# Optimization experiments

Measured on AMD Instinct MI355X. Metric: run time of the kernel, lower is better.

## Reference

```python
import jax, jax.numpy as jnp
import numpy as np

EMB = 512
HEADS = 8
HEAD_DIM = EMB // HEADS


def setup_inputs() -> dict:
    key = jax.random.key(0)
    ks = jax.random.split(key, 6)
    b, t = 2, 4096
    x = jax.random.normal(ks[0], (b, t, EMB), dtype=jnp.float32)
    sc = 1.0 / np.sqrt(HEAD_DIM).astype(np.float32)
    Wq = jax.random.normal(ks[1], (HEAD_DIM, HEAD_DIM), dtype=jnp.float32) * sc
    Wk = jax.random.normal(ks[2], (HEAD_DIM, HEAD_DIM), dtype=jnp.float32) * sc
    Wv = jax.random.normal(ks[3], (HEAD_DIM, HEAD_DIM), dtype=jnp.float32) * sc
    Wu = jax.random.normal(ks[4], (EMB, EMB), dtype=jnp.float32) * (1.0 / np.sqrt(EMB).astype(np.float32))
    bu = jnp.zeros((EMB,), dtype=jnp.float32)
    return {"x": x, "Wq": Wq, "Wk": Wk, "Wv": Wv, "Wu": Wu, "bu": bu}


def reference(x, Wq, Wk, Wv, Wu, bu):
    b, t, e = x.shape
    s = Wq.shape[0]
    h = e // s
    xh = x.reshape(b, t, h, s)
    # torch Linear: y = x @ W.T (no bias for q/k/v)
    q = jnp.einsum('bthd,ed->bthe', xh, Wq)  # e here == s (head dim)
    k = jnp.einsum('bthd,ed->bthe', xh, Wk)
    v = jnp.einsum('bthd,ed->bthe', xh, Wv)
    # full [b,h,t,t] score matrix, scaled by sqrt(emb_dim) as in source
    dot = jnp.einsum('bqhd,bkhd->bhqk', q, k) / (e ** 0.5)
    att = jax.nn.softmax(dot, axis=-1)
    out = jnp.einsum('bhqk,bkhd->bqhd', att, v).reshape(b, t, e)
    return out @ Wu.T + bu
```

## Files before the change

### kernel.cpp

```cpp
#include <hip/hip_runtime.h>
#include <hip/hip_bf16.h>


#define T 4096
#define HEADS 8
#define HD 64
#define EMB 512
#define BATCH 2
#define BH (BATCH * HEADS)
#define NT (T / 64)

typedef __attribute__((ext_vector_type(8))) short short8;
typedef __attribute__((ext_vector_type(4))) short short4v;
typedef __attribute__((ext_vector_type(4))) float floatx4;

__device__ inline short f2bf(float f) {
  union { float f; unsigned u; } v; v.f = f;
  unsigned r = v.u + 0x7FFF + ((v.u >> 16) & 1);
  return (short)(r >> 16);
}

__device__ inline float bf2f(short s) {
  union { unsigned u; float f; } v; v.u = ((unsigned)(unsigned short)s) << 16;
  return v.f;
}

__device__ inline short8 pack8(float4 a, float4 b) {
  union { __hip_bfloat162 h[4]; short8 s; } u;
  float2 t;
  t.x = a.x; t.y = a.y; u.h[0] = __float22bfloat162_rn(t);
  t.x = a.z; t.y = a.w; u.h[1] = __float22bfloat162_rn(t);
  t.x = b.x; t.y = b.y; u.h[2] = __float22bfloat162_rn(t);
  t.x = b.z; t.y = b.w; u.h[3] = __float22bfloat162_rn(t);
  return u.s;
}

__device__ inline short4v pack4(floatx4 a) {
  union { __hip_bfloat162 h[2]; short4v s; } u;
  float2 t;
  t.x = a[0]; t.y = a[1]; u.h[0] = __float22bfloat162_rn(t);
  t.x = a[2]; t.y = a[3]; u.h[1] = __float22bfloat162_rn(t);
  return u.s;
}

__device__ inline short8 packbf(const float* p) {
  union { __hip_bfloat162 h[4]; short8 s; } u;
  float2 t;
  t.x = p[0]; t.y = p[1]; u.h[0] = __float22bfloat162_rn(t);
  t.x = p[2]; t.y = p[3]; u.h[1] = __float22bfloat162_rn(t);
  t.x = p[4]; t.y = p[5]; u.h[2] = __float22bfloat162_rn(t);
  t.x = p[6]; t.y = p[7]; u.h[3] = __float22bfloat162_rn(t);
  return u.s;
}

__device__ inline int swz(int row, int byte) {
  return (row * 128 + byte) ^ ((row & 7) << 4);
}

__device__ inline int swz32(int row, int byte) {
  return (row * 64 + byte) ^ ((row & 3) << 4);
}

__global__ __launch_bounds__(256) void qkv_kernel(
    const float* __restrict__ x, const float* __restrict__ Wq,
    const float* __restrict__ Wk, const float* __restrict__ Wv,
    short* __restrict__ q_ws, short* __restrict__ k_ws, short* __restrict__ vt_ws) {
  __shared__ __align__(16) short xs[128 * 64];
  __shared__ __align__(16) short ob[128 * 64];
  const int tid = threadIdx.x;
  const int lane = tid & 63;
  const int w = tid >> 6;
  const int g = lane >> 4, lr = lane & 15;
  const long rowbase = (long)blockIdx.x * 128;
  const float c2 = 0.0441941738241592f * 1.4426950408889634f;

  {
    int row = tid >> 1, hf = tid & 1;
    const float4* xv = (const float4*)(x + (rowbase + row) * 64 + hf * 32);
#pragma unroll
    for (int c = 0; c < 4; ++c) {
      float4 a = xv[2 * c], b = xv[2 * c + 1];
      *(short8*)((char*)xs + swz(row, hf * 64 + c * 16)) = pack8(a, b);
    }
  }
  __syncthreads();

  const float* Ws[3] = {Wq, Wk, Wv};
  for (int m = 0; m < 3; ++m) {
    const float* W = Ws[m];
    const float sc = (m == 0) ? c2 : 1.0f;
    for (int nt = 0; nt < 4; ++nt) {
      const int coln_a = nt * 16 + lr;
      const float4* wr0 = (const float4*)(W + coln_a * 64 + 8 * g);
      const float4* wr1 = (const float4*)(W + coln_a * 64 + 32 + 8 * g);
      float4 w0 = wr0[0], w1 = wr0[1], w2 = wr1[0], w3 = wr1[1];
      w0.x *= sc; w0.y *= sc; w0.z *= sc; w0.w *= sc;
      w1.x *= sc; w1.y *= sc; w1.z *= sc; w1.w *= sc;
      w2.x *= sc; w2.y *= sc; w2.z *= sc; w2.w *= sc;
      w3.x *= sc; w3.y *= sc; w3.z *= sc; w3.w *= sc;
      short8 b0 = pack8(w0, w1);
      short8 b1 = pack8(w2, w3);
      for (int mr = 0; mr < 2; ++mr) {
        const int arow = w * 32 + mr * 16 + lr;
        short8 a0 = *(short8*)((char*)xs + swz(arow, g * 16));
        short8 a1 = *(short8*)((char*)xs + swz(arow, 64 + g * 16));
        floatx4 acc = 0;
        acc = __builtin_amdgcn_mfma_f32_16x16x32_bf16(b0, a0, acc, 0, 0, 0);
        acc = __builtin_amdgcn_mfma_f32_16x16x32_bf16(b1, a1, acc, 0, 0, 0);
        if (m < 2) {
          *(short4v*)((char*)ob + swz(w * 32 + mr * 16 + lr, 32 * nt + 8 * g)) = pack4(acc);
        } else {
          long R = rowbase + w * 32 + mr * 16 + lr;
          int bb = (int)(R >> 15);
          int h = (int)(R & 7);
          int t = (int)((R >> 3) & 4095);
          int tp = (t & ~31) | (((t >> 2) & 3) << 3) | (((t >> 4) & 1) << 2) | (t & 3);
          short4v pk = pack4(acc);
#pragma unroll
          for (int jj = 0; jj < 4; ++jj) {
            int coln = nt * 16 + 4 * g + jj;
            vt_ws[((long)(bb * HEADS + h) * 64 + coln) * T + tp] = pk[jj];
          }
        }
      }
    }
    if (m < 2) {
      short* dst_ws = (m == 0) ? q_ws : k_ws;
      __syncthreads();
      {
        int row = tid >> 1, hf = tid & 1;
        long R = rowbase + row;
        int bb = (int)(R >> 15);
        int h = (int)(R & 7);
        int t = (int)((R >> 3) & 4095);
        short* dst = dst_ws + ((long)(bb * HEADS + h) * T + t) * 64 + hf * 32;
#pragma unroll
        for (int c = 0; c < 4; ++c) {
          short8 v = *(short8*)((char*)ob + swz(row, hf * 64 + c * 16));
          *(short8*)(dst + c * 8) = v;
        }
      }
      __syncthreads();
    }
  }
}

__global__ __launch_bounds__(256, 4) void attn_kernel(
    const short* __restrict__ q_ws, const short* __restrict__ k_ws,
    const short* __restrict__ vt_ws, short* __restrict__ pacc,
    float* __restrict__ ellw) {
  __shared__ __align__(16) short Ks[32 * 64];
  __shared__ __align__(16) short Vs[64 * 32];
  const int tid = threadIdx.x, lane = tid & 63, w = tid >> 6;
  const int g = lane >> 4, lr = lane & 15;
  const int id = blockIdx.x;
  const int bh = (id & 7) * 2 + ((id >> 3) & 1);
  const int q0 = ((id >> 4) & 31) * 128;
  const int split = (id >> 9) & 3;
  const int kvbase = split * (T / 4);
  const short* Qp = q_ws + (long)bh * T * 64;
  const short* Kp = k_ws + (long)bh * T * 64;
  const short* Vt = vt_ws + (long)bh * 64 * T;

  short8 aq[2][2];
#pragma unroll
  for (int mt = 0; mt < 2; ++mt) {
    int r = q0 + w * 32 + mt * 16 + lr;
    aq[mt][0] = *(const short8*)(Qp + (long)r * 64 + g * 8);
    aq[mt][1] = *(const short8*)(Qp + (long)r * 64 + 32 + g * 8);
  }

  floatx4 acc[2][4];
#pragma unroll
  for (int mt = 0; mt < 2; ++mt)
#pragma unroll
    for (int dt = 0; dt < 4; ++dt) acc[mt][dt] = 0;
  float ellp[2] = {0.f, 0.f};

  const int srowK = tid >> 3;
  const int segK = (tid & 7) * 8;
  const int srowV = tid >> 2;
  const int segV = (tid & 3) * 8;

  {
    short8 k0 = *(const short8*)(Kp + (long)(kvbase + srowK) * 64 + segK);
    short8 v0 = *(const short8*)(Vt + (long)srowV * T + kvbase + segV);
    *(short8*)((char*)Ks + swz(srowK, segK * 2)) = k0;
    *(short8*)((char*)Vs + swz32(srowV, segV * 2)) = v0;
  }
  __syncthreads();

  for (int it = 0; it < 32; ++it) {
    const int nk = kvbase + ((it + 1) & 31) * 32;
    short8 nk0 = *(const short8*)(Kp + (long)(nk + srowK) * 64 + segK);
    short8 nv0 = *(const short8*)(Vt + (long)srowV * T + nk + segV);

    short8 kb[2][2], vb[4];
#pragma unroll
    for (int kt = 0; kt < 2; ++kt) {
      kb[kt][0] = *(const short8*)((char*)Ks + swz(kt * 16 + lr, g * 16));
      kb[kt][1] = *(const short8*)((char*)Ks + swz(kt * 16 + lr, 64 + g * 16));
    }
#pragma unroll
    for (int dt = 0; dt < 4; ++dt)
      vb[dt] = *(const short8*)((char*)Vs + swz32(dt * 16 + lr, g * 16));

#pragma unroll
    for (int mt = 0; mt < 2; ++mt) {
      floatx4 s[2];
#pragma unroll
      for (int kt = 0; kt < 2; ++kt) {
        floatx4 z = {-3.f, -3.f, -3.f, -3.f};
        z = __builtin_amdgcn_mfma_f32_16x16x32_bf16(kb[kt][0], aq[mt][0], z, 0, 0, 0);
        z = __builtin_amdgcn_mfma_f32_16x16x32_bf16(kb[kt][1], aq[mt][1], z, 0, 0, 0);
        s[kt] = z;
      }
      float p[8];
#pragma unroll
      for (int kt = 0; kt < 2; ++kt)
#pragma unroll
        for (int r = 0; r < 4; ++r)
          p[kt * 4 + r] = __builtin_amdgcn_exp2f(s[kt][r]);
#pragma unroll
      for (int e = 0; e < 8; ++e) ellp[mt] += p[e];
      short8 pa = packbf(p);
#pragma unroll
      for (int dt = 0; dt < 4; ++dt)
        acc[mt][dt] = __builtin_amdgcn_mfma_f32_16x16x32_bf16(pa, vb[dt], acc[mt][dt], 0, 0, 0);
    }
    __syncthreads();
    *(short8*)((char*)Ks + swz(srowK, segK * 2)) = nk0;
    *(short8*)((char*)Vs + swz32(srowV, segV * 2)) = nv0;
    __syncthreads();
  }

  float ef[2];
#pragma unroll
  for (int mt = 0; mt < 2; ++mt) {
    float e = ellp[mt];
    e += __shfl_xor(e, 16);
    e += __shfl_xor(e, 32);
    ef[mt] = e;
  }
  const int bb = bh >> 3, h = bh & 7;
  short* pb = pacc + (long)split * 8192 * EMB;
#pragma unroll
  for (int mt = 0; mt < 2; ++mt) {
    if (g == 0)
      ellw[((long)split * BH + bh) * T + q0 + w * 32 + mt * 16 + lr] = ef[mt];
#pragma unroll
    for (int j = 0; j < 4; ++j) {
      int trow = q0 + w * 32 + mt * 16 + 4 * g + j;
      long ob2 = ((long)(bb * T + trow)) * EMB + h * 64;
#pragma unroll
      for (int dt = 0; dt < 4; ++dt)
        pb[ob2 + dt * 16 + lr] = f2bf(acc[mt][dt][j]);
    }
  }
}

__global__ __launch_bounds__(256) void merge_kernel(
    short* __restrict__ pacc, const float* __restrict__ ellw) {
  const long osz = (long)8192 * EMB;
  const long idx = (long)blockIdx.x * 256 + threadIdx.x;
  const long e8 = idx * 8;
  const int r = (int)(e8 >> 9);
  const int c = (int)(e8 & 511);
  const int b = r >> 12, t = r & 4095, h = c >> 6;
  const int bh = b * HEADS + h;
  float l = 0.f;
#pragma unroll
  for (int s = 0; s < 4; ++s) l += ellw[((long)s * BH + bh) * T + t];
  float rl = 1.0f / l;
  float o[8];
#pragma unroll
  for (int i = 0; i < 8; ++i) o[i] = 0.f;
#pragma unroll
  for (int s = 0; s < 4; ++s) {
    short8 p = *(short8*)(pacc + (long)s * osz + e8);
#pragma unroll
    for (int i = 0; i < 8; ++i) o[i] += bf2f(p[i]);
  }
#pragma unroll
  for (int i = 0; i < 8; ++i) o[i] *= rl;
  *(short8*)(pacc + e8) = packbf(o);
}

__global__ __launch_bounds__(256) void proj_kernel(
    const short* __restrict__ o_ws, const float* __restrict__ Wu,
    const float* __restrict__ bu, float* __restrict__ out) {
  __shared__ __align__(16) short As[64 * 64];
  __shared__ __align__(16) short Bs[128 * 64];
  const int tid = threadIdx.x;
  const int lane = tid & 63, w = tid >> 6;
  const int g = lane >> 4, lr = lane & 15;
  const int m0 = blockIdx.x * 64;
  const int n0 = blockIdx.y * 128;

  floatx4 acc[8];
#pragma unroll
  for (int nt = 0; nt < 8; ++nt) acc[nt] = 0;

  for (int kc = 0; kc < EMB; kc += 64) {
    {
      int row = tid >> 2, kp = (tid & 3) * 16;
      const short8* src = (const short8*)(o_ws + (long)(m0 + row) * EMB + kc + kp);
      short8 v0 = src[0], v1 = src[1];
      *(short8*)((char*)As + swz(row, kp * 2)) = v0;
      *(short8*)((char*)As + swz(row, kp * 2 + 16)) = v1;
    }
#pragma unroll
    for (int nn = 0; nn < 2; ++nn) {
      int n = nn * 64 + (tid >> 2), kp = (tid & 3) * 16;
      const float4* src = (const float4*)(Wu + (long)(n0 + n) * EMB + kc + kp);
      *(short8*)((char*)Bs + swz(n, kp * 2)) = pack8(src[0], src[1]);
      *(short8*)((char*)Bs + swz(n, kp * 2 + 16)) = pack8(src[2], src[3]);
    }
    __syncthreads();

    int arow = w * 16 + lr;
    short8 a0 = *(short8*)((char*)As + swz(arow, g * 16));
    short8 a1 = *(short8*)((char*)As + swz(arow, 64 + g * 16));
#pragma unroll
    for (int nt = 0; nt < 8; ++nt) {
      int n = nt * 16 + lr;
      short8 b0 = *(short8*)((char*)Bs + swz(n, g * 16));
      short8 b1 = *(short8*)((char*)Bs + swz(n, 64 + g * 16));
      acc[nt] = __builtin_amdgcn_mfma_f32_16x16x32_bf16(b0, a0, acc[nt], 0, 0, 0);
      acc[nt] = __builtin_amdgcn_mfma_f32_16x16x32_bf16(b1, a1, acc[nt], 0, 0, 0);
    }
    __syncthreads();
  }

  const int mrow = m0 + w * 16 + lr;
#pragma unroll
  for (int nt = 0; nt < 8; ++nt) {
    float4 bias = *(const float4*)(bu + n0 + nt * 16 + 4 * g);
    float4 o;
    o.x = acc[nt][0] + bias.x;
    o.y = acc[nt][1] + bias.y;
    o.z = acc[nt][2] + bias.z;
    o.w = acc[nt][3] + bias.w;
    *(float4*)(out + (long)mrow * EMB + n0 + nt * 16 + 4 * g) = o;
  }
}

extern "C" void kernel_launch(void* const* d_in, const int* in_sizes, int n_in,
                              void* d_out, int out_size, void* d_ws, size_t ws_size,
                              hipStream_t stream) {
  const float* x  = (const float*)d_in[0];
  const float* Wq = (const float*)d_in[1];
  const float* Wk = (const float*)d_in[2];
  const float* Wv = (const float*)d_in[3];
  const float* Wu = (const float*)d_in[4];
  const float* bu = (const float*)d_in[5];
  float* out = (float*)d_out;

  const long per = (long)BH * T * 64;
  const long osz = (long)8192 * EMB;
  short* q_ws  = (short*)d_ws;
  short* k_ws  = q_ws + per;
  short* vt_ws = k_ws + per;
  short* pacc  = vt_ws + per;
  float* ellw  = (float*)(pacc + 4 * osz);

  qkv_kernel<<<512, 256, 0, stream>>>(x, Wq, Wk, Wv, q_ws, k_ws, vt_ws);
  attn_kernel<<<2048, 256, 0, stream>>>(q_ws, k_ws, vt_ws, pacc, ellw);
  merge_kernel<<<(int)(osz / 8 / 256), 256, 0, stream>>>(pacc, ellw);
  proj_kernel<<<dim3(BATCH * T / 64, EMB / 128), 256, 0, stream>>>(pacc, Wu, bu, out);
}
```

Before: 128.8 us.

## Halve KV split count and fuse split merge into projection kernel

```diff
diff --git a/kernel.cpp b/kernel.cpp
--- a/kernel.cpp
+++ b/kernel.cpp
@@ -156,8 +156,8 @@
   const int id = blockIdx.x;
   const int bh = (id & 7) * 2 + ((id >> 3) & 1);
   const int q0 = ((id >> 4) & 31) * 128;
-  const int split = (id >> 9) & 3;
-  const int kvbase = split * (T / 4);
+  const int split = (id >> 9) & 1;
+  const int kvbase = split * (T / 2);
   const short* Qp = q_ws + (long)bh * T * 64;
   const short* Kp = k_ws + (long)bh * T * 64;
   const short* Vt = vt_ws + (long)bh * 64 * T;
@@ -190,8 +190,8 @@
   }
   __syncthreads();
 
-  for (int it = 0; it < 32; ++it) {
-    const int nk = kvbase + ((it + 1) & 31) * 32;
+  for (int it = 0; it < 64; ++it) {
+    const int nk = kvbase + ((it + 1) & 63) * 32;
     short8 nk0 = *(const short8*)(Kp + (long)(nk + srowK) * 64 + segK);
     short8 nv0 = *(const short8*)(Vt + (long)srowV * T + nk + segV);
 
@@ -259,38 +259,13 @@
   }
 }
 
-__global__ __launch_bounds__(256) void merge_kernel(
-    short* __restrict__ pacc, const float* __restrict__ ellw) {
-  const long osz = (long)8192 * EMB;
-  const long idx = (long)blockIdx.x * 256 + threadIdx.x;
-  const long e8 = idx * 8;
-  const int r = (int)(e8 >> 9);
-  const int c = (int)(e8 & 511);
-  const int b = r >> 12, t = r & 4095, h = c >> 6;
-  const int bh = b * HEADS + h;
-  float l = 0.f;
-#pragma unroll
-  for (int s = 0; s < 4; ++s) l += ellw[((long)s * BH + bh) * T + t];
-  float rl = 1.0f / l;
-  float o[8];
-#pragma unroll
-  for (int i = 0; i < 8; ++i) o[i] = 0.f;
-#pragma unroll
-  for (int s = 0; s < 4; ++s) {
-    short8 p = *(short8*)(pacc + (long)s * osz + e8);
-#pragma unroll
-    for (int i = 0; i < 8; ++i) o[i] += bf2f(p[i]);
-  }
-#pragma unroll
-  for (int i = 0; i < 8; ++i) o[i] *= rl;
-  *(short8*)(pacc + e8) = packbf(o);
-}
-
 __global__ __launch_bounds__(256) void proj_kernel(
-    const short* __restrict__ o_ws, const float* __restrict__ Wu,
-    const float* __restrict__ bu, float* __restrict__ out) {
+    const short* __restrict__ pacc, const float* __restrict__ ellw,
+    const float* __restrict__ Wu, const float* __restrict__ bu,
+    float* __restrict__ out) {
   __shared__ __align__(16) short As[64 * 64];
   __shared__ __align__(16) short Bs[128 * 64];
+  const long osz = (long)8192 * EMB;
   const int tid = threadIdx.x;
   const int lane = tid & 63, w = tid >> 6;
   const int g = lane >> 4, lr = lane & 15;
@@ -304,10 +279,23 @@
   for (int kc = 0; kc < EMB; kc += 64) {
     {
       int row = tid >> 2, kp = (tid & 3) * 16;
-      const short8* src = (const short8*)(o_ws + (long)(m0 + row) * EMB + kc + kp);
-      short8 v0 = src[0], v1 = src[1];
-      *(short8*)((char*)As + swz(row, kp * 2)) = v0;
-      *(short8*)((char*)As + swz(row, kp * 2 + 16)) = v1;
+      long R = m0 + row;
+      int bb = (int)(R >> 12), t = (int)(R & 4095);
+      int h = kc >> 6;
+      int bh = bb * HEADS + h;
+      float l = ellw[(long)bh * T + t] + ellw[((long)BH + bh) * T + t];
+      float rl = 1.0f / l;
+      const short8* s0 = (const short8*)(pacc + R * EMB + kc + kp);
+      const short8* s1 = (const short8*)(pacc + osz + R * EMB + kc + kp);
+      short8 p00 = s0[0], p01 = s0[1], p10 = s1[0], p11 = s1[1];
+      float o0[8], o1[8];
+#pragma unroll
+      for (int i = 0; i < 8; ++i) {
+        o0[i] = (bf2f(p00[i]) + bf2f(p10[i])) * rl;
+        o1[i] = (bf2f(p01[i]) + bf2f(p11[i])) * rl;
+      }
+      *(short8*)((char*)As + swz(row, kp * 2)) = packbf(o0);
+      *(short8*)((char*)As + swz(row, kp * 2 + 16)) = packbf(o1);
     }
 #pragma unroll
     for (int nn = 0; nn < 2; ++nn) {
@@ -362,10 +350,9 @@
   short* k_ws  = q_ws + per;
   short* vt_ws = k_ws + per;
   short* pacc  = vt_ws + per;
-  float* ellw  = (float*)(pacc + 4 * osz);
+  float* ellw  = (float*)(pacc + 2 * osz);
 
   qkv_kernel<<<512, 256, 0, stream>>>(x, Wq, Wk, Wv, q_ws, k_ws, vt_ws);
-  attn_kernel<<<2048, 256, 0, stream>>>(q_ws, k_ws, vt_ws, pacc, ellw);
-  merge_kernel<<<(int)(osz / 8 / 256), 256, 0, stream>>>(pacc, ellw);
-  proj_kernel<<<dim3(BATCH * T / 64, EMB / 128), 256, 0, stream>>>(pacc, Wu, bu, out);
-}
+  attn_kernel<<<1024, 256, 0, stream>>>(q_ws, k_ws, vt_ws, pacc, ellw);
+  proj_kernel<<<dim3(BATCH * T / 64, EMB / 128), 256, 0, stream>>>(pacc, ellw, Wu, bu, out);
+}
```

Result: faster. 122.7 us (median of 2 runs) (-4.7%).
